# Performance work log

Hardware: AMD Instinct MI355X
Metric: run time of the kernel (lower is better)

The kernel has to match this reference:

```python
import jax, jax.numpy as jnp
import numpy as np

B, S, D, H = 2, 2048, 1024, 16
DK = D // H


def setup_inputs() -> dict:
    key = jax.random.key(0)
    ks = jax.random.split(key, 12)
    scale = 1.0 / np.sqrt(D)
    inp = {
        "query": jax.random.normal(ks[0], (B, S, D), jnp.float32),
        "key": jax.random.normal(ks[1], (B, S, D), jnp.float32),
        "value": jax.random.normal(ks[2], (B, S, D), jnp.float32),
        "mask": jax.random.randint(ks[3], (B, 1, S, S), 0, 2, jnp.int32),
        "Wq": jax.random.normal(ks[4], (D, D), jnp.float32) * scale,
        "bq": jnp.zeros((D,), jnp.float32),
        "Wk": jax.random.normal(ks[5], (D, D), jnp.float32) * scale,
        "bk": jnp.zeros((D,), jnp.float32),
        "Wv": jax.random.normal(ks[6], (D, D), jnp.float32) * scale,
        "bv": jnp.zeros((D,), jnp.float32),
        "Wo": jax.random.normal(ks[7], (D, D), jnp.float32) * scale,
        "bo": jnp.zeros((D,), jnp.float32),
    }
    return inp


def reference(query, key, value, mask, Wq, bq, Wk, bk, Wv, bv, Wo, bo):
    # Linear projections (dropout is identity in eval mode)
    q = query @ Wq + bq          # (B,S,D)
    k = key @ Wk + bk
    v = value @ Wv + bv

    # split heads: (B,S,D) -> (B,H,S,DK)
    def split(x):
        return x.reshape(B, S, H, DK).transpose(0, 2, 1, 3)

    q, k, v = split(q), split(k), split(v)

    scores = jnp.einsum("bhqd,bhkd->bhqk", q, k) / jnp.sqrt(jnp.float32(DK))
    scores = jnp.where(mask == 0, jnp.float32(-1e9), scores)
    p_attn = jax.nn.softmax(scores, axis=-1)   # (B,H,S,S)

    att = jnp.einsum("bhqk,bhkd->bhqd", p_attn, v)  # (B,H,S,DK)
    merged = att.transpose(0, 2, 1, 3).reshape(B, S, D)
    return merged @ Wo + bo
```

## Files before the change

### kernel.cpp

```cpp
#include <hip/hip_runtime.h>
#include <hip/hip_bf16.h>
#include <cstdint>
#include <cstddef>


#define B_ 2
#define S_ 2048
#define D_ 1024
#define H_ 16
#define M_ 4096

typedef unsigned short u16;
typedef __attribute__((ext_vector_type(8))) short bf16x8;
typedef __attribute__((ext_vector_type(8))) unsigned short u16x8;
typedef __attribute__((ext_vector_type(4))) unsigned short u16x4;
typedef __attribute__((ext_vector_type(4))) unsigned int u32x4;
typedef __attribute__((ext_vector_type(4))) float f32x4;
typedef __attribute__((ext_vector_type(4))) int i32x4;

#define QSCALE 0.18033688011112042f

__device__ __forceinline__ u16 f2bf(float f) {
  __hip_bfloat16 h = __float2bfloat16(f);
  return *reinterpret_cast<u16*>(&h);
}

__device__ __forceinline__ unsigned cvtpk(float lo, float hi) {
  unsigned r;
  asm("v_cvt_pk_bf16_f32 %0, %1, %2" : "=v"(r) : "v"(lo), "v"(hi));
  return r;
}

__device__ __forceinline__ void gload_lds16(const void* g, void* l) {
  __builtin_amdgcn_global_load_lds((const __attribute__((address_space(1))) void*)g,
                                   (__attribute__((address_space(3))) void*)l, 16, 0, 0);
}

__global__ __launch_bounds__(256) void k_transposeW(const float* __restrict__ w0, const float* __restrict__ w1,
                                                    const float* __restrict__ w2, const float* __restrict__ w3,
                                                    u16* __restrict__ t0, u16* __restrict__ t1,
                                                    u16* __restrict__ t2, u16* __restrict__ t3) {
  int z = blockIdx.z;
  const float* W = (z==0)?w0:(z==1)?w1:(z==2)?w2:w3;
  u16* Wt = (z==0)?t0:(z==1)?t1:(z==2)?t2:t3;
  __shared__ float tile[32][33];
  int tx = threadIdx.x & 31, ty = threadIdx.x >> 5;
  int bx = blockIdx.x * 32, by = blockIdx.y * 32;
  #pragma unroll
  for (int p = 0; p < 4; ++p)
    tile[ty + p*8][tx] = W[(size_t)(by + ty + p*8) * D_ + bx + tx];
  __syncthreads();
  #pragma unroll
  for (int p = 0; p < 4; ++p)
    Wt[(size_t)(bx + ty + p*8) * D_ + by + tx] = f2bf(tile[tx][ty + p*8]);
}

__global__ __launch_bounds__(256) void k_packmask(const int* __restrict__ mask, u16* __restrict__ out) {
  size_t t = (size_t)blockIdx.x * 256 + threadIdx.x;
  const int* p = mask + t * 64;
  unsigned wds0 = 0, wds1 = 0, wds2 = 0, wds3 = 0;
  #pragma unroll
  for (int c = 0; c < 16; ++c) {
    i32x4 v = *(const i32x4*)(p + c*4);
    #pragma unroll
    for (int e = 0; e < 4; ++e) {
      const int k = c*4 + e;
      const int lcw = (k >> 3) & 3;
      const int ni = ((k >> 4) & 2) | ((k >> 2) & 1);
      const unsigned bit = 1u << (4*ni + (k & 3));
      if (v[e]) {
        if (lcw == 0) wds0 |= bit; else if (lcw == 1) wds1 |= bit;
        else if (lcw == 2) wds2 |= bit; else wds3 |= bit;
      }
    }
  }
  u16x4 w; w[0] = (u16)wds0; w[1] = (u16)wds1; w[2] = (u16)wds2; w[3] = (u16)wds3;
  *(u16x4*)(out + t*4) = w;
}

template<int CMODE, int MI, int NI, int AF32>
__device__ __forceinline__ void gemm_core(const void* __restrict__ Av, const u16* __restrict__ Bt,
                                          const float* __restrict__ bias, void* __restrict__ Cv,
                                          float scale, int bm, int bn) {
  extern __shared__ u16 sm[];
  constexpr int ASZ = MI*32*64;
  u16* As = sm;
  u16* Bs = sm + ASZ;
  const int t = threadIdx.x;
  const int l = t & 63, w = t >> 6;
  const int wr = w >> 1, wc = w & 1;
  const int lr = l & 15, lc = l >> 4;
  f32x4 acc[MI][NI];
  #pragma unroll
  for (int i = 0; i < MI; ++i)
    #pragma unroll
    for (int j = 0; j < NI; ++j) { f32x4 z = {0.f,0.f,0.f,0.f}; acc[i][j] = z; }
  const int srow = t >> 3;
  const int blkx = (t & 7) ^ (srow & 7);
  const u16*  ga16 = (const u16*)Av  + (size_t)(bm*(MI*32) + srow)*1024 + blkx*8;
  const float* gaf = (const float*)Av + (size_t)(bm*(MI*32) + srow)*1024 + blkx*8;
  const u16* gb = Bt + (size_t)(bn*(NI*32) + srow)*1024 + blkx*8;
  for (int kt = 0; kt < 16; ++kt) {
    const int ko = kt * 64;
    __syncthreads();
    #pragma unroll
    for (int i = 0; i < NI; ++i)
      gload_lds16(gb + (size_t)(i*32)*1024 + ko, &Bs[i*2048 + t*8]);
    if (AF32) {
      f32x4 a0[MI], a1[MI];
      #pragma unroll
      for (int i = 0; i < MI; ++i) {
        a0[i] = *(const f32x4*)(gaf + (size_t)(i*32)*1024 + ko);
        a1[i] = *(const f32x4*)(gaf + (size_t)(i*32)*1024 + ko + 4);
      }
      #pragma unroll
      for (int i = 0; i < MI; ++i) {
        u32x4 wv;
        wv[0] = cvtpk(a0[i][0], a0[i][1]);
        wv[1] = cvtpk(a0[i][2], a0[i][3]);
        wv[2] = cvtpk(a1[i][0], a1[i][1]);
        wv[3] = cvtpk(a1[i][2], a1[i][3]);
        *(u32x4*)&As[i*2048 + t*8] = wv;
      }
    } else {
      #pragma unroll
      for (int i = 0; i < MI; ++i)
        gload_lds16(ga16 + (size_t)(i*32)*1024 + ko, &As[i*2048 + t*8]);
    }
    __syncthreads();
    #pragma unroll
    for (int ks = 0; ks < 2; ++ks) {
      bf16x8 af[MI], bfr[NI];
      #pragma unroll
      for (int mi = 0; mi < MI; ++mi)
        af[mi]  = *(const bf16x8*)&As[(wr*(MI*16) + mi*16 + lr)*64 + (((ks*4 + lc) ^ (lr & 7))*8)];
      #pragma unroll
      for (int ni = 0; ni < NI; ++ni)
        bfr[ni] = *(const bf16x8*)&Bs[(wc*(NI*16) + ni*16 + lr)*64 + (((ks*4 + lc) ^ (lr & 7))*8)];
      #pragma unroll
      for (int mi = 0; mi < MI; ++mi)
        #pragma unroll
        for (int ni = 0; ni < NI; ++ni)
          acc[mi][ni] = __builtin_amdgcn_mfma_f32_16x16x32_bf16(af[mi], bfr[ni], acc[mi][ni], 0, 0, 0);
    }
  }
  #pragma unroll
  for (int ni = 0; ni < NI; ++ni) {
    int gcol = bn*(NI*32) + wc*(NI*16) + ni*16 + lr;
    float bv = bias[gcol];
    #pragma unroll
    for (int mi = 0; mi < MI; ++mi) {
      int grow = bm*(MI*32) + wr*(MI*16) + mi*16 + lc*4;
      if (CMODE == 2) {
        u16x4 pk;
        #pragma unroll
        for (int j = 0; j < 4; ++j) pk[j] = f2bf((acc[mi][ni][j] + bv) * scale);
        *(u16x4*)&((u16*)Cv)[(size_t)gcol * M_ + grow] = pk;
      } else {
        #pragma unroll
        for (int j = 0; j < 4; ++j) {
          float v = (acc[mi][ni][j] + bv) * scale;
          if (CMODE == 0) ((u16*)Cv)[(size_t)(grow + j) * 1024 + gcol] = f2bf(v);
          else            ((float*)Cv)[(size_t)(grow + j) * 1024 + gcol] = v;
        }
      }
    }
  }
}

__global__ __launch_bounds__(256, 4) void k_gemm_qkv(const float* q, const float* k, const float* v,
                                                     const u16* Wqt, const u16* Wkt, const u16* Wvt,
                                                     const float* bq, const float* bk, const float* bv,
                                                     u16* Qo, u16* Ko, u16* Vt, float qscale) {
  const int id = blockIdx.x + (blockIdx.y << 5) + (blockIdx.z << 8);
  const int lg = (id & 7) * 96 + (id >> 3);
  const int bm = lg & 31;
  const int panel = lg >> 5;
  const int bn = panel & 7, z = panel >> 3;
  if (z == 0)      gemm_core<0,4,4,1>(q, Wqt, bq, Qo, qscale, bm, bn);
  else if (z == 1) gemm_core<0,4,4,1>(k, Wkt, bk, Ko, 1.f,    bm, bn);
  else             gemm_core<2,4,4,1>(v, Wvt, bv, Vt, 1.f,    bm, bn);
}

__global__ __launch_bounds__(256, 4) void k_gemm_out(const u16* Aatt, const u16* Wot, const float* bo, float* out) {
  const int id = blockIdx.x + (blockIdx.y << 5);
  const int lg = (id & 7) * 64 + (id >> 3);
  const int bm = lg & 31, bn = lg >> 5;
  gemm_core<1,4,2,0>(Aatt, Wot, bo, out, 1.f, bm, bn);
}

__global__ __launch_bounds__(512, 4) void k_attn(const u16* __restrict__ Q, const u16* __restrict__ Kb,
                                                 const u16* __restrict__ Vt,
                                                 const u16* __restrict__ mbw,
                                                 u16* __restrict__ attb) {
  __shared__ u16 Ks[3*4096];
  __shared__ u16 Vs[2*4096];
  const int t = threadIdx.x, l = t & 63, w = t >> 6;
  const int lr = l & 15, lc = l >> 4;
  const int id = blockIdx.x + (blockIdx.y << 4) + (blockIdx.z << 8);
  const int lg = (id & 7) * 64 + (id >> 3);
  const int qt = lg & 15, h = (lg >> 4) & 15, b = lg >> 8;
  const int r0 = t >> 3;
  const int c0 = (t & 7) ^ (r0 & 7);
  const int pr0 = (r0 & 32) | ((r0 & 12) << 1) | ((r0 & 16) >> 2) | (r0 & 3);
  const u16* kp0 = Kb + (size_t)(b*S_ + pr0)*D_ + h*64 + c0*8;
  const u16* vp0 = Vt + (size_t)(h*64 + r0)*M_ + b*S_ + c0*8;

  gload_lds16(Q + (size_t)(b*S_ + qt*128 + r0)*D_      + h*64 + c0*8, &Ks[t*8]);
  gload_lds16(Q + (size_t)(b*S_ + qt*128 + 64 + r0)*D_ + h*64 + c0*8, &Ks[4096 + t*8]);
  __syncthreads();
  const int qrow = w*16 + lr;
  const int sw0 = ((lc     ) ^ (lr & 7)) * 8;
  const int sw1 = ((4 + lc ) ^ (lr & 7)) * 8;
  const int qbuf = (qrow >> 6) * 4096, qrl = (qrow & 63) * 64;
  bf16x8 aq0 = *(const bf16x8*)&Ks[qbuf + qrl + sw0];
  bf16x8 aq1 = *(const bf16x8*)&Ks[qbuf + qrl + sw1];
  __syncthreads();
  gload_lds16(kp0,                  &Ks[t*8]);
  gload_lds16(vp0,                  &Vs[t*8]);
  gload_lds16(kp0 + (size_t)64*D_,  &Ks[4096 + t*8]);

  const short one_bf = (short)0x3F80;
  const bf16x8 onesf = {one_bf,one_bf,one_bf,one_bf,one_bf,one_bf,one_bf,one_bf};
  f32x4 ls = {0.f,0.f,0.f,0.f};
  f32x4 o[4];
  #pragma unroll
  for (int ni = 0; ni < 4; ++ni) { f32x4 z = {0.f,0.f,0.f,0.f}; o[ni] = z; }
  const u16* mkp = mbw + (size_t)(b*S_ + qt*128 + qrow)*128 + lc;
  const u16* vpA = vp0;
  const u16* kpA = kp0;

#define AITER(N, KC, VC, VN, KNN, KPRE, VPRE, WAITN) {                                 \
    asm volatile("s_waitcnt vmcnt(" #WAITN ")");                                       \
    __builtin_amdgcn_s_barrier();                                                      \
    __builtin_amdgcn_sched_barrier(0);                                                 \
    unsigned mw = mkp[(N)*4];                                                          \
    if (VPRE) gload_lds16(vpA + ((N)+1)*64,              &Vs[(VN)*4096 + t*8]);        \
    if (KPRE) gload_lds16(kpA + (size_t)((N)+2)*64*D_,   &Ks[(KNN)*4096 + t*8]);       \
    f32x4 s[4];                                                                        \
    _Pragma("unroll")                                                                  \
    for (int ni = 0; ni < 4; ++ni) { f32x4 z = {0.f,0.f,0.f,0.f}; s[ni] = z; }         \
    __builtin_amdgcn_s_setprio(1);                                                     \
    _Pragma("unroll")                                                                  \
    for (int ni = 0; ni < 4; ++ni) {                                                   \
      bf16x8 bk0 = *(const bf16x8*)&Ks[(KC)*4096 + (ni*16 + lr)*64 + sw0];             \
      bf16x8 bk1 = *(const bf16x8*)&Ks[(KC)*4096 + (ni*16 + lr)*64 + sw1];             \
      s[ni] = __builtin_amdgcn_mfma_f32_16x16x32_bf16(bk0, aq0, s[ni], 0, 0, 0);       \
      s[ni] = __builtin_amdgcn_mfma_f32_16x16x32_bf16(bk1, aq1, s[ni], 0, 0, 0);       \
    }                                                                                  \
    __builtin_amdgcn_s_setprio(0);                                                     \
    _Pragma("unroll")                                                                  \
    for (int ni = 0; ni < 4; ++ni)                                                     \
      _Pragma("unroll")                                                                \
      for (int j = 0; j < 4; ++j) {                                                    \
        float pv = __builtin_amdgcn_exp2f(s[ni][j]);                                   \
        int bmsk = ((int)(mw << (31 - (4*ni + j)))) >> 31;                             \
        union { float f; int i; } u; u.f = pv; u.i &= bmsk;                            \
        s[ni][j] = u.f;                                                                \
      }                                                                                \
    u32x4 pw0, pw1;                                                                    \
    pw0[0] = cvtpk(s[0][0], s[0][1]); pw0[1] = cvtpk(s[0][2], s[0][3]);                \
    pw0[2] = cvtpk(s[1][0], s[1][1]); pw0[3] = cvtpk(s[1][2], s[1][3]);                \
    pw1[0] = cvtpk(s[2][0], s[2][1]); pw1[1] = cvtpk(s[2][2], s[2][3]);                \
    pw1[2] = cvtpk(s[3][0], s[3][1]); pw1[3] = cvtpk(s[3][2], s[3][3]);                \
    bf16x8 pa0 = __builtin_bit_cast(bf16x8, pw0);                                      \
    bf16x8 pa1 = __builtin_bit_cast(bf16x8, pw1);                                      \
    __builtin_amdgcn_s_setprio(1);                                                     \
    ls = __builtin_amdgcn_mfma_f32_16x16x32_bf16(pa0, onesf, ls, 0, 0, 0);             \
    ls = __builtin_amdgcn_mfma_f32_16x16x32_bf16(pa1, onesf, ls, 0, 0, 0);             \
    _Pragma("unroll")                                                                  \
    for (int ni = 0; ni < 4; ++ni) {                                                   \
      bf16x8 bv0 = *(const bf16x8*)&Vs[(VC)*4096 + (ni*16 + lr)*64 + sw0];             \
      o[ni] = __builtin_amdgcn_mfma_f32_16x16x32_bf16(pa0, bv0, o[ni], 0, 0, 0);       \
    }                                                                                  \
    _Pragma("unroll")                                                                  \
    for (int ni = 0; ni < 4; ++ni) {                                                   \
      bf16x8 bv1 = *(const bf16x8*)&Vs[(VC)*4096 + (ni*16 + lr)*64 + sw1];             \
      o[ni] = __builtin_amdgcn_mfma_f32_16x16x32_bf16(pa1, bv1, o[ni], 0, 0, 0);       \
    }                                                                                  \
    __builtin_amdgcn_s_setprio(0);                                                     \
  }

  for (int it = 0; it < 5; ++it) {
    AITER(0, 0,0, 1,2, 1,1, 1);
    AITER(1, 1,1, 0,0, 1,1, 1);
    AITER(2, 2,0, 1,1, 1,1, 1);
    AITER(3, 0,1, 0,2, 1,1, 1);
    AITER(4, 1,0, 1,0, 1,1, 1);
    AITER(5, 2,1, 0,1, 1,1, 1);
    mkp += 24;
    vpA += 6*64;
    kpA += (size_t)6*64*D_;
  }
  AITER(0, 0,0, 1,0, 0,1, 1);
  AITER(1, 1,1, 0,0, 0,0, 0);
#undef AITER

  float rl[4];
  #pragma unroll
  for (int j = 0; j < 4; ++j) rl[j] = 1.f / ls[j];
  #pragma unroll
  for (int ni = 0; ni < 4; ++ni)
    #pragma unroll
    for (int j = 0; j < 4; ++j) {
      int orow = qt*128 + w*16 + lc*4 + j, dcol = ni*16 + lr;
      attb[(size_t)(b*S_ + orow)*D_ + h*64 + dcol] = f2bf(o[ni][j] * rl[j]);
    }
}

extern "C" void kernel_launch(void* const* d_in, const int* in_sizes, int n_in,
                              void* d_out, int out_size, void* d_ws, size_t ws_size,
                              hipStream_t stream) {
  (void)in_sizes; (void)n_in; (void)out_size; (void)ws_size;
  const float* query = (const float*)d_in[0];
  const float* key   = (const float*)d_in[1];
  const float* value = (const float*)d_in[2];
  const int*   mask  = (const int*)d_in[3];
  const float* Wq = (const float*)d_in[4];
  const float* bq = (const float*)d_in[5];
  const float* Wk = (const float*)d_in[6];
  const float* bk = (const float*)d_in[7];
  const float* Wv = (const float*)d_in[8];
  const float* bv = (const float*)d_in[9];
  const float* Wo = (const float*)d_in[10];
  const float* bo = (const float*)d_in[11];
  float* out = (float*)d_out;
  char* ws = (char*)d_ws;
  const size_t MB = 1024 * 1024;
  u16* Wqt = (u16*)(ws + 24*MB);
  u16* Wkt = (u16*)(ws + 26*MB);
  u16* Wvt = (u16*)(ws + 28*MB);
  u16* Wot = (u16*)(ws + 30*MB);
  u16* Qb  = (u16*)(ws + 32*MB);
  u16* Kb  = (u16*)(ws + 40*MB);
  u16* Vtb = (u16*)(ws + 48*MB);
  u16* mbits = (u16*)(ws + 56*MB);
  u16* attb = (u16*)(ws + 0*MB);

  k_transposeW<<<dim3(32, 32, 4),  256, 0,     stream>>>(Wq, Wk, Wv, Wo, Wqt, Wkt, Wvt, Wot);
  k_packmask <<<dim3(512),         256, 0,     stream>>>(mask, mbits);
  k_gemm_qkv <<<dim3(32, 8, 3),    256, 32768, stream>>>(query, key, value, Wqt, Wkt, Wvt,
                                                         bq, bk, bv, Qb, Kb, Vtb, QSCALE);
  k_attn     <<<dim3(16, 16, 2),   512, 0,     stream>>>(Qb, Kb, Vtb, mbits, attb);
  k_gemm_out <<<dim3(32, 16),      256, 24576, stream>>>(attb, Wot, bo, out);
}
```

Before: 134.3 us.

## Register-prefetch next K tile in QKV GEMM and split out-proj GEMM

The QKV projection GEMM now loads the next K-slice of fp32 activations and bf16 weights into registers while the MFMAs on the current LDS tile run. Weights go through registers instead of direct global-to-LDS loads. This is meant to hide global load latency behind compute, and the MFMA block is wrapped in s_setprio. The price is more registers, so launch bounds drop to 3 blocks per SM. The output GEMM is split into its own specialized kernel with the same logic as before, plus restrict qualifiers.

```diff
diff --git a/kernel.cpp b/kernel.cpp
--- a/kernel.cpp
+++ b/kernel.cpp
@@ -78,79 +78,81 @@
   *(u16x4*)(out + t*4) = w;
 }
 
-template<int CMODE, int MI, int NI, int AF32>
-__device__ __forceinline__ void gemm_core(const void* __restrict__ Av, const u16* __restrict__ Bt,
-                                          const float* __restrict__ bias, void* __restrict__ Cv,
-                                          float scale, int bm, int bn) {
+template<int CMODE>
+__device__ __forceinline__ void gemm_qkv_core(const float* __restrict__ A, const u16* __restrict__ Bt,
+                                              const float* __restrict__ bias, void* __restrict__ Cv,
+                                              float scale, int bm, int bn) {
   extern __shared__ u16 sm[];
-  constexpr int ASZ = MI*32*64;
   u16* As = sm;
-  u16* Bs = sm + ASZ;
+  u16* Bs = sm + 8192;
   const int t = threadIdx.x;
   const int l = t & 63, w = t >> 6;
   const int wr = w >> 1, wc = w & 1;
   const int lr = l & 15, lc = l >> 4;
-  f32x4 acc[MI][NI];
-  #pragma unroll
-  for (int i = 0; i < MI; ++i)
-    #pragma unroll
-    for (int j = 0; j < NI; ++j) { f32x4 z = {0.f,0.f,0.f,0.f}; acc[i][j] = z; }
+  f32x4 acc[4][4];
+  #pragma unroll
+  for (int i = 0; i < 4; ++i)
+    #pragma unroll
+    for (int j = 0; j < 4; ++j) { f32x4 z = {0.f,0.f,0.f,0.f}; acc[i][j] = z; }
   const int srow = t >> 3;
   const int blkx = (t & 7) ^ (srow & 7);
-  const u16*  ga16 = (const u16*)Av  + (size_t)(bm*(MI*32) + srow)*1024 + blkx*8;
-  const float* gaf = (const float*)Av + (size_t)(bm*(MI*32) + srow)*1024 + blkx*8;
-  const u16* gb = Bt + (size_t)(bn*(NI*32) + srow)*1024 + blkx*8;
+  const float* ga = A  + (size_t)(bm*128 + srow)*1024 + blkx*8;
+  const u16*   gb = Bt + (size_t)(bn*128 + srow)*1024 + blkx*8;
+  f32x4 a0[4], a1[4];
+  u16x8 brg[4];
+  #pragma unroll
+  for (int i = 0; i < 4; ++i) {
+    a0[i]  = *(const f32x4*)(ga + (size_t)(i*32)*1024);
+    a1[i]  = *(const f32x4*)(ga + (size_t)(i*32)*1024 + 4);
+    brg[i] = *(const u16x8*)(gb + (size_t)(i*32)*1024);
+  }
   for (int kt = 0; kt < 16; ++kt) {
-    const int ko = kt * 64;
     __syncthreads();
     #pragma unroll
-    for (int i = 0; i < NI; ++i)
-      gload_lds16(gb + (size_t)(i*32)*1024 + ko, &Bs[i*2048 + t*8]);
-    if (AF32) {
-      f32x4 a0[MI], a1[MI];
-      #pragma unroll
-      for (int i = 0; i < MI; ++i) {
-        a0[i] = *(const f32x4*)(gaf + (size_t)(i*32)*1024 + ko);
-        a1[i] = *(const f32x4*)(gaf + (size_t)(i*32)*1024 + ko + 4);
+    for (int i = 0; i < 4; ++i) {
+      u32x4 wv;
+      wv[0] = cvtpk(a0[i][0], a0[i][1]);
+      wv[1] = cvtpk(a0[i][2], a0[i][3]);
+      wv[2] = cvtpk(a1[i][0], a1[i][1]);
+      wv[3] = cvtpk(a1[i][2], a1[i][3]);
+      *(u32x4*)&As[i*2048 + t*8] = wv;
+      *(u16x8*)&Bs[i*2048 + t*8] = brg[i];
+    }
+    __syncthreads();
+    if (kt < 15) {
+      const int ko = (kt + 1) * 64;
+      #pragma unroll
+      for (int i = 0; i < 4; ++i) {
+        a0[i]  = *(const f32x4*)(ga + (size_t)(i*32)*1024 + ko);
+        a1[i]  = *(const f32x4*)(ga + (size_t)(i*32)*1024 + ko + 4);
+        brg[i] = *(const u16x8*)(gb + (size_t)(i*32)*1024 + ko);
       }
-      #pragma unroll
-      for (int i = 0; i < MI; ++i) {
-        u32x4 wv;
-        wv[0] = cvtpk(a0[i][0], a0[i][1]);
-        wv[1] = cvtpk(a0[i][2], a0[i][3]);
-        wv[2] = cvtpk(a1[i][0], a1[i][1]);
-        wv[3] = cvtpk(a1[i][2], a1[i][3]);
-        *(u32x4*)&As[i*2048 + t*8] = wv;
-      }
-    } else {
-      #pragma unroll
-      for (int i = 0; i < MI; ++i)
-        gload_lds16(ga16 + (size_t)(i*32)*1024 + ko, &As[i*2048 + t*8]);
-    }
-    __syncthreads();
+    }
     #pragma unroll
     for (int ks = 0; ks < 2; ++ks) {
-      bf16x8 af[MI], bfr[NI];
-      #pragma unroll
-      for (int mi = 0; mi < MI; ++mi)
-        af[mi]  = *(const bf16x8*)&As[(wr*(MI*16) + mi*16 + lr)*64 + (((ks*4 + lc) ^ (lr & 7))*8)];
-      #pragma unroll
-      for (int ni = 0; ni < NI; ++ni)
-        bfr[ni] = *(const bf16x8*)&Bs[(wc*(NI*16) + ni*16 + lr)*64 + (((ks*4 + lc) ^ (lr & 7))*8)];
-      #pragma unroll
-      for (int mi = 0; mi < MI; ++mi)
+      bf16x8 af[4], bfr[4];
+      #pragma unroll
+      for (int mi = 0; mi < 4; ++mi)
+        af[mi]  = *(const bf16x8*)&As[(wr*64 + mi*16 + lr)*64 + (((ks*4 + lc) ^ (lr & 7))*8)];
+      #pragma unroll
+      for (int ni = 0; ni < 4; ++ni)
+        bfr[ni] = *(const bf16x8*)&Bs[(wc*64 + ni*16 + lr)*64 + (((ks*4 + lc) ^ (lr & 7))*8)];
+      __builtin_amdgcn_s_setprio(1);
+      #pragma unroll
+      for (int mi = 0; mi < 4; ++mi)
         #pragma unroll
-        for (int ni = 0; ni < NI; ++ni)
+        for (int ni = 0; ni < 4; ++ni)
           acc[mi][ni] = __builtin_amdgcn_mfma_f32_16x16x32_bf16(af[mi], bfr[ni], acc[mi][ni], 0, 0, 0);
-    }
-  }
-  #pragma unroll
-  for (int ni = 0; ni < NI; ++ni) {
-    int gcol = bn*(NI*32) + wc*(NI*16) + ni*16 + lr;
+      __builtin_amdgcn_s_setprio(0);
+    }
+  }
+  #pragma unroll
+  for (int ni = 0; ni < 4; ++ni) {
+    int gcol = bn*128 + wc*64 + ni*16 + lr;
     float bv = bias[gcol];
     #pragma unroll
-    for (int mi = 0; mi < MI; ++mi) {
-      int grow = bm*(MI*32) + wr*(MI*16) + mi*16 + lc*4;
+    for (int mi = 0; mi < 4; ++mi) {
+      int grow = bm*128 + wr*64 + mi*16 + lc*4;
       if (CMODE == 2) {
         u16x4 pk;
         #pragma unroll
@@ -158,17 +160,14 @@
         *(u16x4*)&((u16*)Cv)[(size_t)gcol * M_ + grow] = pk;
       } else {
         #pragma unroll
-        for (int j = 0; j < 4; ++j) {
-          float v = (acc[mi][ni][j] + bv) * scale;
-          if (CMODE == 0) ((u16*)Cv)[(size_t)(grow + j) * 1024 + gcol] = f2bf(v);
-          else            ((float*)Cv)[(size_t)(grow + j) * 1024 + gcol] = v;
-        }
+        for (int j = 0; j < 4; ++j)
+          ((u16*)Cv)[(size_t)(grow + j) * 1024 + gcol] = f2bf((acc[mi][ni][j] + bv) * scale);
       }
     }
   }
 }
 
-__global__ __launch_bounds__(256, 4) void k_gemm_qkv(const float* q, const float* k, const float* v,
+__global__ __launch_bounds__(256, 3) void k_gemm_qkv(const float* q, const float* k, const float* v,
                                                      const u16* Wqt, const u16* Wkt, const u16* Wvt,
                                                      const float* bq, const float* bk, const float* bv,
                                                      u16* Qo, u16* Ko, u16* Vt, float qscale) {
@@ -177,16 +176,70 @@
   const int bm = lg & 31;
   const int panel = lg >> 5;
   const int bn = panel & 7, z = panel >> 3;
-  if (z == 0)      gemm_core<0,4,4,1>(q, Wqt, bq, Qo, qscale, bm, bn);
-  else if (z == 1) gemm_core<0,4,4,1>(k, Wkt, bk, Ko, 1.f,    bm, bn);
-  else             gemm_core<2,4,4,1>(v, Wvt, bv, Vt, 1.f,    bm, bn);
-}
-
-__global__ __launch_bounds__(256, 4) void k_gemm_out(const u16* Aatt, const u16* Wot, const float* bo, float* out) {
+  if (z == 0)      gemm_qkv_core<0>(q, Wqt, bq, Qo, qscale, bm, bn);
+  else if (z == 1) gemm_qkv_core<0>(k, Wkt, bk, Ko, 1.f,    bm, bn);
+  else             gemm_qkv_core<2>(v, Wvt, bv, Vt, 1.f,    bm, bn);
+}
+
+__global__ __launch_bounds__(256, 4) void k_gemm_out(const u16* __restrict__ Aatt, const u16* __restrict__ Wot,
+                                                     const float* __restrict__ bo, float* __restrict__ out) {
+  extern __shared__ u16 sm[];
+  u16* As = sm;
+  u16* Bs = sm + 8192;
   const int id = blockIdx.x + (blockIdx.y << 5);
   const int lg = (id & 7) * 64 + (id >> 3);
   const int bm = lg & 31, bn = lg >> 5;
-  gemm_core<1,4,2,0>(Aatt, Wot, bo, out, 1.f, bm, bn);
+  const int t = threadIdx.x;
+  const int l = t & 63, w = t >> 6;
+  const int wr = w >> 1, wc = w & 1;
+  const int lr = l & 15, lc = l >> 4;
+  f32x4 acc[4][2];
+  #pragma unroll
+  for (int i = 0; i < 4; ++i)
+    #pragma unroll
+    for (int j = 0; j < 2; ++j) { f32x4 z = {0.f,0.f,0.f,0.f}; acc[i][j] = z; }
+  const int srow = t >> 3;
+  const int blkx = (t & 7) ^ (srow & 7);
+  const u16* ga = Aatt + (size_t)(bm*128 + srow)*1024 + blkx*8;
+  const u16* gb = Wot  + (size_t)(bn*64  + srow)*1024 + blkx*8;
+  for (int kt = 0; kt < 16; ++kt) {
+    const int ko = kt * 64;
+    __syncthreads();
+    #pragma unroll
+    for (int i = 0; i < 4; ++i)
+      gload_lds16(ga + (size_t)(i*32)*1024 + ko, &As[i*2048 + t*8]);
+    #pragma unroll
+    for (int i = 0; i < 2; ++i)
+      gload_lds16(gb + (size_t)(i*32)*1024 + ko, &Bs[i*2048 + t*8]);
+    __syncthreads();
+    #pragma unroll
+    for (int ks = 0; ks < 2; ++ks) {
+      bf16x8 af[4], bfr[2];
+      #pragma unroll
+      for (int mi = 0; mi < 4; ++mi)
+        af[mi]  = *(const bf16x8*)&As[(wr*64 + mi*16 + lr)*64 + (((ks*4 + lc) ^ (lr & 7))*8)];
+      #pragma unroll
+      for (int ni = 0; ni < 2; ++ni)
+        bfr[ni] = *(const bf16x8*)&Bs[(wc*32 + ni*16 + lr)*64 + (((ks*4 + lc) ^ (lr & 7))*8)];
+      #pragma unroll
+      for (int mi = 0; mi < 4; ++mi)
+        #pragma unroll
+        for (int ni = 0; ni < 2; ++ni)
+          acc[mi][ni] = __builtin_amdgcn_mfma_f32_16x16x32_bf16(af[mi], bfr[ni], acc[mi][ni], 0, 0, 0);
+    }
+  }
+  #pragma unroll
+  for (int ni = 0; ni < 2; ++ni) {
+    int gcol = bn*64 + wc*32 + ni*16 + lr;
+    float bv = bo[gcol];
+    #pragma unroll
+    for (int mi = 0; mi < 4; ++mi) {
+      int grow = bm*128 + wr*64 + mi*16 + lc*4;
+      #pragma unroll
+      for (int j = 0; j < 4; ++j)
+        out[(size_t)(grow + j) * 1024 + gcol] = acc[mi][ni][j] + bv;
+    }
+  }
 }
 
 __global__ __launch_bounds__(512, 4) void k_attn(const u16* __restrict__ Q, const u16* __restrict__ Kb,
```

New measurement: 142.7 us. +6.2%, slower.
